# Kernel optimization log

Hardware: AMD Instinct MI355X
Metric: run time of the kernel (lower is better)

The kernel has to match this reference:

```python
import jax, jax.numpy as jnp
import numpy as np

N = 100000
E = 3200000
IN_CH, HID, OUT = 256, 64, 32


def setup_inputs() -> dict:
    key = jax.random.key(0)
    ks = jax.random.split(key, 8)
    x = jax.random.normal(ks[0], (N, IN_CH), dtype=jnp.float32)
    edge_index = jax.random.randint(ks[1], (2, E), 0, N, dtype=jnp.int64)
    # Glorot-ish init for weights, zeros for biases (PyG GCNConv: lin has no bias; conv bias added post-aggregation)
    W1 = jax.random.normal(ks[2], (IN_CH, HID), dtype=jnp.float32) / np.sqrt(IN_CH)
    b1 = jnp.zeros((HID,), dtype=jnp.float32)
    W2 = jax.random.normal(ks[3], (HID, OUT), dtype=jnp.float32) / np.sqrt(HID)
    b2 = jnp.zeros((OUT,), dtype=jnp.float32)
    Wc = jax.random.normal(ks[4], (OUT, 1), dtype=jnp.float32) / np.sqrt(OUT)
    bc = jnp.zeros((1,), dtype=jnp.float32)
    return {"x": x, "edge_index": edge_index, "W1": W1, "b1": b1,
            "W2": W2, "b2": b2, "Wc": Wc, "bc": bc}


def _gcn_norm(edge_index, num_nodes):
    # Add self-loops (PyG default), compute symmetric normalization D^{-1/2} A D^{-1/2}
    loops = jnp.arange(num_nodes, dtype=edge_index.dtype)
    row = jnp.concatenate([edge_index[0], loops])  # source
    col = jnp.concatenate([edge_index[1], loops])  # target (aggregation index)
    ones = jnp.ones(row.shape[0], dtype=jnp.float32)
    deg = jax.ops.segment_sum(ones, col, num_segments=num_nodes)
    dis = jnp.where(deg > 0, jax.lax.rsqrt(jnp.maximum(deg, 1e-12)), 0.0)
    norm = dis[row] * dis[col]  # [E+N]
    return row, col, norm


def _gcn_conv(x, W, b, row, col, norm, num_nodes):
    h = x @ W                                   # [N, F_out] dense transform first
    msg = h[row] * norm[:, None]                # gather + scale per edge
    agg = jax.ops.segment_sum(msg, col, num_segments=num_nodes)
    return agg + b


def reference(x, edge_index, W1, b1, W2, b2, Wc, bc):
    num_nodes = x.shape[0]
    row, col, norm = _gcn_norm(edge_index, num_nodes)
    h = jax.nn.elu(_gcn_conv(x, W1, b1, row, col, norm, num_nodes))
    h = jax.nn.elu(_gcn_conv(h, W2, b2, row, col, norm, num_nodes))
    return (h @ Wc + bc)[:, 0]                  # squeeze(1) -> [N]
```

## Files before the change

### kernel.cpp

```cpp
#include <hip/hip_runtime.h>
#include <hip/hip_fp16.h>
#include <math.h>

#define N_NODES 100000
#define N_EDGES 3200000
#define IN_CH   256
#define HID     64
#define OUTC    32
#define BSHIFT  7
#define BNODES  128
#define NBUCK   ((N_NODES + BNODES - 1) / BNODES)
#define CHUNK   4096
#define EPT     16
#define CAP     4608
#define NPART   ((N_EDGES + CHUNK - 1) / CHUNK)
#define NG1     ((N_NODES + 127) / 128)

static constexpr size_t align256(size_t x) { return (x + 255) & ~(size_t)255; }
static constexpr size_t OFF_PTRB = 0;
static constexpr size_t OFF_PTRE = OFF_PTRB + align256((size_t)N_NODES * 4);
static constexpr size_t OFF_GCUR = OFF_PTRE + align256((size_t)N_NODES * 4);
static constexpr size_t OFF_DIS  = OFF_GCUR + align256((size_t)NBUCK * 4);
static constexpr size_t OFF_SRC  = OFF_DIS  + align256((size_t)N_NODES * 4);
static constexpr size_t OFF_PART = OFF_SRC  + align256((size_t)NBUCK * CAP * 4);
static constexpr size_t OFF_S1   = OFF_PART + align256((size_t)NBUCK * CAP * 4);
static constexpr size_t OFF_S2   = OFF_S1   + align256((size_t)N_NODES * HID * 2);

typedef _Float16 f16;
typedef f16 f16x8 __attribute__((ext_vector_type(8)));
typedef float f32x4 __attribute__((ext_vector_type(4)));

__device__ __forceinline__ void acc8(float* acc, float4 raw) {
    const __half2* hp = (const __half2*)&raw;
    float2 f0 = __half22float2(hp[0]);
    float2 f1 = __half22float2(hp[1]);
    float2 f2 = __half22float2(hp[2]);
    float2 f3 = __half22float2(hp[3]);
    acc[0] += f0.x; acc[1] += f0.y; acc[2] += f1.x; acc[3] += f1.y;
    acc[4] += f2.x; acc[5] += f2.y; acc[6] += f3.x; acc[7] += f3.y;
}


__device__ __forceinline__ void partition_body(int pb, const int* __restrict__ row,
                                               const int* __restrict__ col,
                                               int* __restrict__ gcur,
                                               int* __restrict__ part,
                                               char* smem) {
    int* lhist = (int*)smem;
    int* lbase = lhist + NBUCK;
    const int t  = threadIdx.x;
    const int e0 = pb * CHUNK;
    for (int i = t; i < NBUCK; i += 256) lhist[i] = 0;
    __syncthreads();

    int pk[EPT], br[EPT];
#pragma unroll
    for (int i = 0; i < EPT; ++i) {
        int e = e0 + i * 256 + t;
        if (e < N_EDGES) {
            int d = col[e];
            int b = d >> BSHIFT;
            int r = atomicAdd(&lhist[b], 1);
            pk[i] = row[e] | ((d & (BNODES - 1)) << 17);
            br[i] = b | (r << 10);
        } else {
            br[i] = -1;
        }
    }
    __syncthreads();

    const int off = (int)((pb * 131u) % NBUCK);
    for (int i = t; i < NBUCK; i += 256) {
        int bb = i + off;
        if (bb >= NBUCK) bb -= NBUCK;
        int c = lhist[bb];
        lbase[bb] = (c > 0) ? atomicAdd(&gcur[bb], c) : 0;
    }
    __syncthreads();

#pragma unroll
    for (int i = 0; i < EPT; ++i) {
        if (br[i] >= 0) {
            int b = br[i] & 1023;
            int r = br[i] >> 10;
            part[b * CAP + lbase[b] + r] = pk[i];
        }
    }
}

__device__ __forceinline__ void gemm1_body(int gb, const float* __restrict__ x,
                                           const float* __restrict__ W1,
                                           __half* __restrict__ s1h,
                                           char* lds_raw) {
    f16* xh  = (f16*)lds_raw;
    f16* xl  = (f16*)(lds_raw + 10240);
    f16* wth = (f16*)(lds_raw + 20480);
    f16* wtl = (f16*)(lds_raw + 25600);

    const int t    = threadIdx.x;
    const int row0 = gb * 128;
    const int lane = t & 63;
    const int wv   = t >> 6;
    const int lr   = lane & 15;
    const int kg   = lane >> 4;

    f32x4 acc[2][4];
#pragma unroll
    for (int m = 0; m < 2; ++m)
#pragma unroll
        for (int n = 0; n < 4; ++n) acc[m][n] = (f32x4){0.f, 0.f, 0.f, 0.f};

    for (int kt = 0; kt < 8; ++kt) {
#pragma unroll
        for (int i = 0; i < 4; ++i) {
            int L  = i * 256 + t;
            int r  = L >> 3;
            int k4 = L & 7;
            int rg = row0 + r;
            float4 v = make_float4(0.f, 0.f, 0.f, 0.f);
            if (rg < N_NODES)
                v = ((const float4*)x)[(size_t)rg * 64 + kt * 8 + k4];
            union { f16 h[4]; unsigned long long u; } ph, pl;
            const float* vf = (const float*)&v;
#pragma unroll
            for (int c = 0; c < 4; ++c) {
                f16 hi = (f16)vf[c];
                ph.h[c] = hi;
                pl.h[c] = (f16)(vf[c] - (float)hi);
            }
            *(unsigned long long*)(&xh[r * 40 + k4 * 4]) = ph.u;
            *(unsigned long long*)(&xl[r * 40 + k4 * 4]) = pl.u;
        }
#pragma unroll
        for (int i = 0; i < 2; ++i) {
            int L  = i * 256 + t;
            int k  = L >> 4;
            int j4 = L & 15;
            float4 v = ((const float4*)W1)[(size_t)(kt * 32 + k) * 16 + j4];
            const float* vf = (const float*)&v;
#pragma unroll
            for (int c = 0; c < 4; ++c) {
                f16 hi = (f16)vf[c];
                wth[(j4 * 4 + c) * 40 + k] = hi;
                wtl[(j4 * 4 + c) * 40 + k] = (f16)(vf[c] - (float)hi);
            }
        }
        __syncthreads();

        f16x8 ah[2], al[2], bh[4], bl[4];
#pragma unroll
        for (int m = 0; m < 2; ++m) {
            ah[m] = *(const f16x8*)(&xh[(wv * 32 + m * 16 + lr) * 40 + kg * 8]);
            al[m] = *(const f16x8*)(&xl[(wv * 32 + m * 16 + lr) * 40 + kg * 8]);
        }
#pragma unroll
        for (int n = 0; n < 4; ++n) {
            bh[n] = *(const f16x8*)(&wth[(n * 16 + lr) * 40 + kg * 8]);
            bl[n] = *(const f16x8*)(&wtl[(n * 16 + lr) * 40 + kg * 8]);
        }
#pragma unroll
        for (int m = 0; m < 2; ++m)
#pragma unroll
            for (int n = 0; n < 4; ++n) {
                acc[m][n] = __builtin_amdgcn_mfma_f32_16x16x32_f16(ah[m], bh[n], acc[m][n], 0, 0, 0);
                acc[m][n] = __builtin_amdgcn_mfma_f32_16x16x32_f16(ah[m], bl[n], acc[m][n], 0, 0, 0);
                acc[m][n] = __builtin_amdgcn_mfma_f32_16x16x32_f16(al[m], bh[n], acc[m][n], 0, 0, 0);
            }
        __syncthreads();
    }

    f16* ob = (f16*)lds_raw;
#pragma unroll
    for (int m = 0; m < 2; ++m) {
#pragma unroll
        for (int r = 0; r < 4; ++r) {
            int rl = wv * 32 + m * 16 + kg * 4 + r;
#pragma unroll
            for (int n = 0; n < 4; ++n)
                ob[rl * 72 + n * 16 + lr] = (f16)(acc[m][n][r]);
        }
    }
    __syncthreads();
#pragma unroll
    for (int i = 0; i < 4; ++i) {
        int L = i * 256 + t;
        int r = L >> 3;
        int sg = L & 7;
        int rg = row0 + r;
        if (rg < N_NODES) {
            f16x8 v = *(const f16x8*)(&ob[r * 72 + sg * 8]);
            *(f16x8*)(s1h + (size_t)rg * HID + sg * 8) = v;
        }
    }
}

__global__ __launch_bounds__(256) void fused_pg(const int* __restrict__ row,
                                                const int* __restrict__ col,
                                                int* __restrict__ gcur,
                                                int* __restrict__ part,
                                                const float* __restrict__ x,
                                                const float* __restrict__ W1,
                                                __half* __restrict__ s1h) {
    __shared__ __align__(16) char smem[30720];
    const int bid = blockIdx.x;
    if (bid & 1) gemm1_body(bid >> 1, x, W1, s1h, smem);
    else         partition_body(bid >> 1, row, col, gcur, part, smem);
}

__global__ __launch_bounds__(512) void bucket_build(const int* __restrict__ gcur,
                                                    const int* __restrict__ part,
                                                    int* __restrict__ ptrb,
                                                    int* __restrict__ ptre,
                                                    float* __restrict__ dis,
                                                    int* __restrict__ srcs,
                                                    __half* __restrict__ s1h) {
    __shared__ int pcache[CAP];
    __shared__ int lh[BNODES];
    __shared__ int lb[BNODES];
    __shared__ int lcur[BNODES];
    __shared__ int ls[BNODES];
    __shared__ float ldis[BNODES];
    const int b = blockIdx.x;
    const int t = threadIdx.x;
    if (t < BNODES) { lh[t] = 0; lcur[t] = 0; }
    __syncthreads();
    const int cnt = gcur[b];
    const size_t pbase = (size_t)b * CAP;

    for (int i = t; i < cnt; i += 512) {
        int p = part[pbase + i];
        pcache[i] = p;
        atomicAdd(&lh[p >> 17], 1);
    }
    __syncthreads();

    int val = (t < BNODES) ? lh[t] : 0;
    if (t < BNODES) ls[t] = val;
    __syncthreads();
    for (int off = 1; off < BNODES; off <<= 1) {
        int add = (t >= off && t < BNODES) ? ls[t - off] : 0;
        __syncthreads();
        if (t < BNODES) ls[t] += add;
        __syncthreads();
    }
    if (t < BNODES) lb[t] = ls[t] - val;
    __syncthreads();

    int v = b * BNODES + t;
    if (t < BNODES) {
        float d = rsqrtf((float)val + 1.0f);
        ldis[t] = d;
        if (v < N_NODES) {
            ptrb[v] = b * CAP + lb[t];
            ptre[v] = b * CAP + lb[t] + val;
            dis[v]  = d;
        }
    }
    __syncthreads();

    for (int i = t; i < cnt; i += 512) {
        int p    = pcache[i];
        int dlow = p >> 17;
        int src  = p & 0x1FFFF;
        int r    = atomicAdd(&lcur[dlow], 1);
        srcs[pbase + lb[dlow] + r] = src;
    }

    {
        int nrows = N_NODES - b * BNODES;
        if (nrows > BNODES) nrows = BNODES;
        const int nwork = nrows * 8;
        for (int i = t; i < nwork; i += 512) {
            int r  = i >> 3;
            int sg = i & 7;
            __half* p = s1h + (size_t)(b * BNODES + r) * HID + sg * 8;
            f16x8 vv = *(const f16x8*)p;
            float d = ldis[r];
            f16x8 ov;
#pragma unroll
            for (int c = 0; c < 8; ++c) ov[c] = (f16)((float)vv[c] * d);
            *(f16x8*)p = ov;
        }
    }
}

__global__ __launch_bounds__(256) void gather1(const __half* __restrict__ s1h,
                                               const int* __restrict__ ptrb,
                                               const int* __restrict__ ptre,
                                               const int* __restrict__ srcs,
                                               const float* __restrict__ dis,
                                               const float* __restrict__ b1,
                                               const float* __restrict__ W2,
                                               __half* __restrict__ s2h) {
    __shared__ float w2lds[HID * OUTC];
    __shared__ float hbuf[4][HID];

    const int t = threadIdx.x;
    {
        float4* l4 = (float4*)w2lds;
        const float4* s4 = (const float4*)W2;
        l4[t] = s4[t];
        l4[256 + t] = s4[256 + t];
    }
    __syncthreads();

    const int j = t & 63;
    const int w = t >> 6;
    const int l = j & 31;
    const int h = j >> 5;
    const int v = __builtin_amdgcn_readfirstlane(blockIdx.x * 4 + w);
    const __half2* s12 = (const __half2*)s1h;

    float2 acc;
    {
        float2 self = __half22float2(s12[(v << 5) | l]);
        acc = (h == 0) ? self : make_float2(0.f, 0.f);
    }
    const int beg = ptrb[v];
    const int end = ptre[v];

    for (int base = beg; base < end; base += 64) {
        int mysrc = 0;
        if (base + j < end) mysrc = srcs[base + j];
        int nk = end - base;
        if (nk > 64) nk = 64;
        const int full = nk >> 1;
        int i = 0;
        for (; i + 8 <= full; i += 8) {
            int s  = 2 * i + h;
            int a0 = __shfl(mysrc, s,      64);
            int a1 = __shfl(mysrc, s + 2,  64);
            int a2 = __shfl(mysrc, s + 4,  64);
            int a3 = __shfl(mysrc, s + 6,  64);
            int a4 = __shfl(mysrc, s + 8,  64);
            int a5 = __shfl(mysrc, s + 10, 64);
            int a6 = __shfl(mysrc, s + 12, 64);
            int a7 = __shfl(mysrc, s + 14, 64);
            float2 g0 = __half22float2(s12[(a0 << 5) | l]);
            float2 g1 = __half22float2(s12[(a1 << 5) | l]);
            float2 g2 = __half22float2(s12[(a2 << 5) | l]);
            float2 g3 = __half22float2(s12[(a3 << 5) | l]);
            float2 g4 = __half22float2(s12[(a4 << 5) | l]);
            float2 g5 = __half22float2(s12[(a5 << 5) | l]);
            float2 g6 = __half22float2(s12[(a6 << 5) | l]);
            float2 g7 = __half22float2(s12[(a7 << 5) | l]);
            acc.x += ((g0.x + g1.x) + (g2.x + g3.x)) + ((g4.x + g5.x) + (g6.x + g7.x));
            acc.y += ((g0.y + g1.y) + (g2.y + g3.y)) + ((g4.y + g5.y) + (g6.y + g7.y));
        }
        if (2 * i < nk) {
            const int last = nk - 1;
#pragma unroll
            for (int u = 0; u < 8; ++u) {
                int s  = 2 * (i + u) + h;
                int sc = s < last ? s : last;
                int a  = __shfl(mysrc, sc, 64);
                float wgt = (s < nk) ? 1.f : 0.f;
                float2 g = __half22float2(s12[(a << 5) | l]);
                acc.x = fmaf(wgt, g.x, acc.x);
                acc.y = fmaf(wgt, g.y, acc.y);
            }
        }
    }
    acc.x += __shfl_xor(acc.x, 32, 64);
    acc.y += __shfl_xor(acc.y, 32, 64);

    float dv = dis[v];
    float2 bb = *(const float2*)(b1 + 2 * l);
    float t0 = dv * acc.x + bb.x;
    float t1 = dv * acc.y + bb.y;
    float h0 = t0 > 0.f ? t0 : (expf(t0) - 1.f);
    float h1 = t1 > 0.f ? t1 : (expf(t1) - 1.f);
    if (h == 0) {
        hbuf[w][2 * l]     = h0;
        hbuf[w][2 * l + 1] = h1;
    }

    const int jo = j & 31;
    const int kb = (j >> 5) * 32;
    float p = 0.f;
#pragma unroll
    for (int kk = 0; kk < 32; ++kk)
        p += hbuf[w][kb + kk] * w2lds[(kb + kk) * OUTC + jo];
    p += __shfl_xor(p, 32, 64);
    if (j < 32) {
        s2h[(size_t)v * OUTC + jo] = __float2half(dv * p);
    }
}

__global__ __launch_bounds__(256) void gather2(const __half* __restrict__ s2h,
                                               const int* __restrict__ ptrb,
                                               const int* __restrict__ ptre,
                                               const int* __restrict__ srcs,
                                               const float* __restrict__ dis,
                                               const float* __restrict__ b2,
                                               const float* __restrict__ Wc,
                                               const float* __restrict__ bc,
                                               float* __restrict__ out) {
    const int j = threadIdx.x & 63;
    const int w = threadIdx.x >> 6;
    const int l = j & 3;
    const int e = j >> 2;
    const int v = __builtin_amdgcn_readfirstlane(blockIdx.x * 4 + w);
    const float4* s24 = (const float4*)s2h;

    float acc[8] = {0.f, 0.f, 0.f, 0.f, 0.f, 0.f, 0.f, 0.f};
    if (e == 0) acc8(acc, s24[(v << 2) | l]);

    const int beg = ptrb[v];
    const int end = ptre[v];
    for (int base = beg; base < end; base += 64) {
        int mys = 0;
        if (base + j < end) mys = srcs[base + j];
        int nk = end - base;
        if (nk > 64) nk = 64;
        int off = 0;
        for (; off + 32 <= nk; off += 32) {
            int a0 = __shfl(mys, off + e,      64);
            int a1 = __shfl(mys, off + 16 + e, 64);
            float4 r0 = s24[(a0 << 2) | l];
            float4 r1 = s24[(a1 << 2) | l];
            acc8(acc, r0);
            acc8(acc, r1);
        }
        if (off < nk) {
            const int last = nk - 1;
            int s0 = off + e, s1 = off + 16 + e;
            int a0 = __shfl(mys, s0 < last ? s0 : last, 64);
            int a1 = __shfl(mys, s1 < last ? s1 : last, 64);
            if (s0 < nk) acc8(acc, s24[(a0 << 2) | l]);
            if (s1 < nk) acc8(acc, s24[(a1 << 2) | l]);
        }
    }
#pragma unroll
    for (int i = 0; i < 8; ++i) {
        acc[i] += __shfl_xor(acc[i], 4, 64);
        acc[i] += __shfl_xor(acc[i], 8, 64);
        acc[i] += __shfl_xor(acc[i], 16, 64);
        acc[i] += __shfl_xor(acc[i], 32, 64);
    }

    float dv = dis[v];
    float4 ba = ((const float4*)b2)[2 * l];
    float4 bb = ((const float4*)b2)[2 * l + 1];
    float4 wa = ((const float4*)Wc)[2 * l];
    float4 wb = ((const float4*)Wc)[2 * l + 1];
    const float* bf = (const float*)&ba;
    const float* bg = (const float*)&bb;
    const float* wf = (const float*)&wa;
    const float* wg = (const float*)&wb;
    float p = 0.f;
#pragma unroll
    for (int i = 0; i < 8; ++i) {
        float bias = (i < 4) ? bf[i] : bg[i - 4];
        float wc   = (i < 4) ? wf[i] : wg[i - 4];
        float tt = dv * acc[i] + bias;
        float hh = tt > 0.f ? tt : (expf(tt) - 1.f);
        p += hh * wc;
    }
    p += __shfl_xor(p, 1, 64);
    p += __shfl_xor(p, 2, 64);
    if (j == 0) out[v] = p + bc[0];
}

extern "C" void kernel_launch(void* const* d_in, const int* in_sizes, int n_in,
                              void* d_out, int out_size, void* d_ws, size_t ws_size,
                              hipStream_t stream) {
    const float* x  = (const float*)d_in[0];
    const int*   ei = (const int*)d_in[1];
    const float* W1 = (const float*)d_in[2];
    const float* b1 = (const float*)d_in[3];
    const float* W2 = (const float*)d_in[4];
    const float* b2 = (const float*)d_in[5];
    const float* Wc = (const float*)d_in[6];
    const float* bc = (const float*)d_in[7];
    float* out = (float*)d_out;

    const int* row = ei;
    const int* col = ei + N_EDGES;

    char* ws = (char*)d_ws;
    int*    ptrb = (int*)   (ws + OFF_PTRB);
    int*    ptre = (int*)   (ws + OFF_PTRE);
    int*    gcur = (int*)   (ws + OFF_GCUR);
    float*  dis  = (float*) (ws + OFF_DIS);
    int*    srcs = (int*)   (ws + OFF_SRC);
    int*    part = (int*)   (ws + OFF_PART);
    __half* s1h  = (__half*)(ws + OFF_S1);
    __half* s2h  = (__half*)(ws + OFF_S2);

    hipMemsetAsync(gcur, 0, (size_t)NBUCK * 4, stream);
    fused_pg    <<<NPART + NG1, 256, 0, stream>>>(row, col, gcur, part, x, W1, s1h);
    bucket_build<<<NBUCK, 512, 0, stream>>>(gcur, part, ptrb, ptre, dis, srcs, s1h);

    gather1<<<N_NODES / 4, 256, 0, stream>>>(s1h, ptrb, ptre, srcs, dis, b1, W2, s2h);
    gather2<<<N_NODES / 4, 256, 0, stream>>>(s2h, ptrb, ptre, srcs, dis, b2, Wc, bc, out);
}
```

Measured before the change: 363.2 us.

## Fuse bucket build and both gather passes into one cooperative persistent kernel

Replaces the separate bucket_build, gather1 and gather2 launches with a single cooperative persistent kernel. Phases are separated by grid-wide syncs, and each phase uses grid-stride loops over buckets and nodes. The bucket build now uses per-wave histograms so the LDS atomics contend less. This removes two kernel launch boundaries and tail effects. In exchange it adds grid-sync cost, and the grid is capped at 1024 blocks of 512 threads with launch bounds of 6, which may limit occupancy for the latency-bound gathers.

```diff
diff --git a/kernel.cpp b/kernel.cpp
--- a/kernel.cpp
+++ b/kernel.cpp
@@ -1,6 +1,9 @@
 #include <hip/hip_runtime.h>
+#include <hip/hip_cooperative_groups.h>
 #include <hip/hip_fp16.h>
 #include <math.h>
+
+namespace cg = cooperative_groups;
 
 #define N_NODES 100000
 #define N_EDGES 3200000
@@ -40,7 +43,6 @@
     acc[4] += f2.x; acc[5] += f2.y; acc[6] += f3.x; acc[7] += f3.y;
 }
 
-
 __device__ __forceinline__ void partition_body(int pb, const int* __restrict__ row,
                                                const int* __restrict__ col,
                                                int* __restrict__ gcur,
@@ -207,259 +209,260 @@
     else         partition_body(bid >> 1, row, col, gcur, part, smem);
 }
 
-__global__ __launch_bounds__(512) void bucket_build(const int* __restrict__ gcur,
-                                                    const int* __restrict__ part,
-                                                    int* __restrict__ ptrb,
-                                                    int* __restrict__ ptre,
-                                                    float* __restrict__ dis,
-                                                    int* __restrict__ srcs,
-                                                    __half* __restrict__ s1h) {
-    __shared__ int pcache[CAP];
-    __shared__ int lh[BNODES];
-    __shared__ int lb[BNODES];
-    __shared__ int lcur[BNODES];
-    __shared__ int ls[BNODES];
-    __shared__ float ldis[BNODES];
-    const int b = blockIdx.x;
-    const int t = threadIdx.x;
-    if (t < BNODES) { lh[t] = 0; lcur[t] = 0; }
+__global__ __launch_bounds__(512, 6) void tail_fused(
+        const int* __restrict__ gcur, const int* __restrict__ part,
+        int* __restrict__ ptrb, int* __restrict__ ptre,
+        float* __restrict__ dis, int* __restrict__ srcs,
+        __half* __restrict__ s1h, __half* __restrict__ s2h,
+        const float* __restrict__ b1, const float* __restrict__ W2,
+        const float* __restrict__ b2, const float* __restrict__ Wc,
+        const float* __restrict__ bc, float* __restrict__ out) {
+    __shared__ __align__(16) char sm[27776];
+    int*   pcache = (int*)sm;
+    int*   wh     = (int*)(sm + 18432);
+    int*   wpre   = (int*)(sm + 22656);
+    int*   lsm    = (int*)(sm + 26752);
+    float* ldis   = (float*)(sm + 27264);
+    float* w2lds  = (float*)sm;
+    float* hbuf   = (float*)(sm + 8192);
+
+    const int t  = threadIdx.x;
+    const int wv = t >> 6;
+    const int j  = t & 63;
+
+    for (int b = blockIdx.x; b < NBUCK; b += gridDim.x) {
+        const int cnt = gcur[b];
+        const size_t pbase = (size_t)b * CAP;
+
+        for (int i = t; i < 8 * 132; i += 512) wh[i] = 0;
+        __syncthreads();
+
+        for (int i = t; i < cnt; i += 512) {
+            int p = part[pbase + i];
+            pcache[i] = p;
+            atomicAdd(&wh[wv * 132 + (p >> 17)], 1);
+        }
+        __syncthreads();
+
+        int val = 0, lbv = 0;
+        if (t < BNODES) {
+            int s = 0;
+#pragma unroll
+            for (int q = 0; q < 8; ++q) { wpre[q * 128 + t] = s; s += wh[q * 132 + t]; }
+            val = s;
+            lsm[t] = s;
+        }
+        __syncthreads();
+        for (int off = 1; off < BNODES; off <<= 1) {
+            int add = (t >= off && t < BNODES) ? lsm[t - off] : 0;
+            __syncthreads();
+            if (t < BNODES) lsm[t] += add;
+            __syncthreads();
+        }
+        if (t < BNODES) {
+            lbv = lsm[t] - val;
+            float d = rsqrtf((float)val + 1.0f);
+            ldis[t] = d;
+            int v = b * BNODES + t;
+            if (v < N_NODES) {
+                ptrb[v] = b * CAP + lbv;
+                ptre[v] = b * CAP + lbv + val;
+                dis[v]  = d;
+            }
+#pragma unroll
+            for (int q = 0; q < 8; ++q) wh[q * 132 + t] = lbv + wpre[q * 128 + t];
+        }
+        __syncthreads();
+
+        for (int i = t; i < cnt; i += 512) {
+            int p    = pcache[i];
+            int dlow = p >> 17;
+            int r    = atomicAdd(&wh[wv * 132 + dlow], 1);
+            srcs[pbase + r] = p & 0x1FFFF;
+        }
+
+        {
+            int base_node = b * BNODES;
+            int nrows = N_NODES - base_node;
+            if (nrows > BNODES) nrows = BNODES;
+            int nwork = nrows * 8;
+            for (int i = t; i < nwork; i += 512) {
+                int r  = i >> 3;
+                int sg = i & 7;
+                f16x8* pp = (f16x8*)(s1h + (size_t)(base_node + r) * HID + sg * 8);
+                f16x8 vv = *pp;
+                float d = ldis[r];
+                f16x8 ov;
+#pragma unroll
+                for (int c = 0; c < 8; ++c) ov[c] = (f16)((float)vv[c] * d);
+                *pp = ov;
+            }
+        }
+        __syncthreads();
+    }
+
+    __threadfence();
+    cg::this_grid().sync();
+
+    {
+        const float4* s4 = (const float4*)W2;
+        if (t < 512) ((float4*)w2lds)[t] = s4[t];
+    }
     __syncthreads();
-    const int cnt = gcur[b];
-    const size_t pbase = (size_t)b * CAP;
-
-    for (int i = t; i < cnt; i += 512) {
-        int p = part[pbase + i];
-        pcache[i] = p;
-        atomicAdd(&lh[p >> 17], 1);
-    }
-    __syncthreads();
-
-    int val = (t < BNODES) ? lh[t] : 0;
-    if (t < BNODES) ls[t] = val;
-    __syncthreads();
-    for (int off = 1; off < BNODES; off <<= 1) {
-        int add = (t >= off && t < BNODES) ? ls[t - off] : 0;
-        __syncthreads();
-        if (t < BNODES) ls[t] += add;
-        __syncthreads();
-    }
-    if (t < BNODES) lb[t] = ls[t] - val;
-    __syncthreads();
-
-    int v = b * BNODES + t;
-    if (t < BNODES) {
-        float d = rsqrtf((float)val + 1.0f);
-        ldis[t] = d;
-        if (v < N_NODES) {
-            ptrb[v] = b * CAP + lb[t];
-            ptre[v] = b * CAP + lb[t] + val;
-            dis[v]  = d;
-        }
-    }
-    __syncthreads();
-
-    for (int i = t; i < cnt; i += 512) {
-        int p    = pcache[i];
-        int dlow = p >> 17;
-        int src  = p & 0x1FFFF;
-        int r    = atomicAdd(&lcur[dlow], 1);
-        srcs[pbase + lb[dlow] + r] = src;
-    }
 
     {
-        int nrows = N_NODES - b * BNODES;
-        if (nrows > BNODES) nrows = BNODES;
-        const int nwork = nrows * 8;
-        for (int i = t; i < nwork; i += 512) {
-            int r  = i >> 3;
-            int sg = i & 7;
-            __half* p = s1h + (size_t)(b * BNODES + r) * HID + sg * 8;
-            f16x8 vv = *(const f16x8*)p;
-            float d = ldis[r];
-            f16x8 ov;
-#pragma unroll
-            for (int c = 0; c < 8; ++c) ov[c] = (f16)((float)vv[c] * d);
-            *(f16x8*)p = ov;
-        }
-    }
-}
-
-__global__ __launch_bounds__(256) void gather1(const __half* __restrict__ s1h,
-                                               const int* __restrict__ ptrb,
-                                               const int* __restrict__ ptre,
-                                               const int* __restrict__ srcs,
-                                               const float* __restrict__ dis,
-                                               const float* __restrict__ b1,
-                                               const float* __restrict__ W2,
-                                               __half* __restrict__ s2h) {
-    __shared__ float w2lds[HID * OUTC];
-    __shared__ float hbuf[4][HID];
-
-    const int t = threadIdx.x;
+        const int l = j & 31;
+        const int h = j >> 5;
+        const __half2* s12 = (const __half2*)s1h;
+        const int nw = gridDim.x * 8;
+        for (int vv = blockIdx.x * 8 + wv; vv < N_NODES; vv += nw) {
+            const int v = __builtin_amdgcn_readfirstlane(vv);
+            float2 acc;
+            {
+                float2 self = __half22float2(s12[(v << 5) | l]);
+                acc = (h == 0) ? self : make_float2(0.f, 0.f);
+            }
+            const int beg = ptrb[v];
+            const int end = ptre[v];
+
+            for (int base = beg; base < end; base += 64) {
+                int mysrc = 0;
+                if (base + j < end) mysrc = srcs[base + j];
+                int nk = end - base;
+                if (nk > 64) nk = 64;
+                const int full = nk >> 1;
+                int i = 0;
+                for (; i + 8 <= full; i += 8) {
+                    int s  = 2 * i + h;
+                    int a0 = __shfl(mysrc, s,      64);
+                    int a1 = __shfl(mysrc, s + 2,  64);
+                    int a2 = __shfl(mysrc, s + 4,  64);
+                    int a3 = __shfl(mysrc, s + 6,  64);
+                    int a4 = __shfl(mysrc, s + 8,  64);
+                    int a5 = __shfl(mysrc, s + 10, 64);
+                    int a6 = __shfl(mysrc, s + 12, 64);
+                    int a7 = __shfl(mysrc, s + 14, 64);
+                    float2 g0 = __half22float2(s12[(a0 << 5) | l]);
+                    float2 g1 = __half22float2(s12[(a1 << 5) | l]);
+                    float2 g2 = __half22float2(s12[(a2 << 5) | l]);
+                    float2 g3 = __half22float2(s12[(a3 << 5) | l]);
+                    float2 g4 = __half22float2(s12[(a4 << 5) | l]);
+                    float2 g5 = __half22float2(s12[(a5 << 5) | l]);
+                    float2 g6 = __half22float2(s12[(a6 << 5) | l]);
+                    float2 g7 = __half22float2(s12[(a7 << 5) | l]);
+                    acc.x += ((g0.x + g1.x) + (g2.x + g3.x)) + ((g4.x + g5.x) + (g6.x + g7.x));
+                    acc.y += ((g0.y + g1.y) + (g2.y + g3.y)) + ((g4.y + g5.y) + (g6.y + g7.y));
+                }
+                if (2 * i < nk) {
+                    const int last = nk - 1;
+#pragma unroll
+                    for (int u = 0; u < 8; ++u) {
+                        int s  = 2 * (i + u) + h;
+                        int sc = s < last ? s : last;
+                        int a  = __shfl(mysrc, sc, 64);
+                        float wgt = (s < nk) ? 1.f : 0.f;
+                        float2 g = __half22float2(s12[(a << 5) | l]);
+                        acc.x = fmaf(wgt, g.x, acc.x);
+                        acc.y = fmaf(wgt, g.y, acc.y);
+                    }
+                }
+            }
+            acc.x += __shfl_xor(acc.x, 32, 64);
+            acc.y += __shfl_xor(acc.y, 32, 64);
+
+            float dv = dis[v];
+            float2 bb = *(const float2*)(b1 + 2 * l);
+            float t0 = dv * acc.x + bb.x;
+            float t1 = dv * acc.y + bb.y;
+            float h0 = t0 > 0.f ? t0 : (expf(t0) - 1.f);
+            float h1 = t1 > 0.f ? t1 : (expf(t1) - 1.f);
+            if (h == 0) {
+                hbuf[wv * HID + 2 * l]     = h0;
+                hbuf[wv * HID + 2 * l + 1] = h1;
+            }
+
+            const int jo = j & 31;
+            const int kb = (j >> 5) * 32;
+            float p = 0.f;
+#pragma unroll
+            for (int kk = 0; kk < 32; ++kk)
+                p += hbuf[wv * HID + kb + kk] * w2lds[(kb + kk) * OUTC + jo];
+            p += __shfl_xor(p, 32, 64);
+            if (j < 32) {
+                s2h[(size_t)v * OUTC + jo] = __float2half(dv * p);
+            }
+        }
+    }
+
+    __threadfence();
+    cg::this_grid().sync();
+
     {
-        float4* l4 = (float4*)w2lds;
-        const float4* s4 = (const float4*)W2;
-        l4[t] = s4[t];
-        l4[256 + t] = s4[256 + t];
-    }
-    __syncthreads();
-
-    const int j = t & 63;
-    const int w = t >> 6;
-    const int l = j & 31;
-    const int h = j >> 5;
-    const int v = __builtin_amdgcn_readfirstlane(blockIdx.x * 4 + w);
-    const __half2* s12 = (const __half2*)s1h;
-
-    float2 acc;
-    {
-        float2 self = __half22float2(s12[(v << 5) | l]);
-        acc = (h == 0) ? self : make_float2(0.f, 0.f);
-    }
-    const int beg = ptrb[v];
-    const int end = ptre[v];
-
-    for (int base = beg; base < end; base += 64) {
-        int mysrc = 0;
-        if (base + j < end) mysrc = srcs[base + j];
-        int nk = end - base;
-        if (nk > 64) nk = 64;
-        const int full = nk >> 1;
-        int i = 0;
-        for (; i + 8 <= full; i += 8) {
-            int s  = 2 * i + h;
-            int a0 = __shfl(mysrc, s,      64);
-            int a1 = __shfl(mysrc, s + 2,  64);
-            int a2 = __shfl(mysrc, s + 4,  64);
-            int a3 = __shfl(mysrc, s + 6,  64);
-            int a4 = __shfl(mysrc, s + 8,  64);
-            int a5 = __shfl(mysrc, s + 10, 64);
-            int a6 = __shfl(mysrc, s + 12, 64);
-            int a7 = __shfl(mysrc, s + 14, 64);
-            float2 g0 = __half22float2(s12[(a0 << 5) | l]);
-            float2 g1 = __half22float2(s12[(a1 << 5) | l]);
-            float2 g2 = __half22float2(s12[(a2 << 5) | l]);
-            float2 g3 = __half22float2(s12[(a3 << 5) | l]);
-            float2 g4 = __half22float2(s12[(a4 << 5) | l]);
-            float2 g5 = __half22float2(s12[(a5 << 5) | l]);
-            float2 g6 = __half22float2(s12[(a6 << 5) | l]);
-            float2 g7 = __half22float2(s12[(a7 << 5) | l]);
-            acc.x += ((g0.x + g1.x) + (g2.x + g3.x)) + ((g4.x + g5.x) + (g6.x + g7.x));
-            acc.y += ((g0.y + g1.y) + (g2.y + g3.y)) + ((g4.y + g5.y) + (g6.y + g7.y));
-        }
-        if (2 * i < nk) {
-            const int last = nk - 1;
-#pragma unroll
-            for (int u = 0; u < 8; ++u) {
-                int s  = 2 * (i + u) + h;
-                int sc = s < last ? s : last;
-                int a  = __shfl(mysrc, sc, 64);
-                float wgt = (s < nk) ? 1.f : 0.f;
-                float2 g = __half22float2(s12[(a << 5) | l]);
-                acc.x = fmaf(wgt, g.x, acc.x);
-                acc.y = fmaf(wgt, g.y, acc.y);
-            }
-        }
-    }
-    acc.x += __shfl_xor(acc.x, 32, 64);
-    acc.y += __shfl_xor(acc.y, 32, 64);
-
-    float dv = dis[v];
-    float2 bb = *(const float2*)(b1 + 2 * l);
-    float t0 = dv * acc.x + bb.x;
-    float t1 = dv * acc.y + bb.y;
-    float h0 = t0 > 0.f ? t0 : (expf(t0) - 1.f);
-    float h1 = t1 > 0.f ? t1 : (expf(t1) - 1.f);
-    if (h == 0) {
-        hbuf[w][2 * l]     = h0;
-        hbuf[w][2 * l + 1] = h1;
-    }
-
-    const int jo = j & 31;
-    const int kb = (j >> 5) * 32;
-    float p = 0.f;
-#pragma unroll
-    for (int kk = 0; kk < 32; ++kk)
-        p += hbuf[w][kb + kk] * w2lds[(kb + kk) * OUTC + jo];
-    p += __shfl_xor(p, 32, 64);
-    if (j < 32) {
-        s2h[(size_t)v * OUTC + jo] = __float2half(dv * p);
-    }
-}
-
-__global__ __launch_bounds__(256) void gather2(const __half* __restrict__ s2h,
-                                               const int* __restrict__ ptrb,
-                                               const int* __restrict__ ptre,
-                                               const int* __restrict__ srcs,
-                                               const float* __restrict__ dis,
-                                               const float* __restrict__ b2,
-                                               const float* __restrict__ Wc,
-                                               const float* __restrict__ bc,
-                                               float* __restrict__ out) {
-    const int j = threadIdx.x & 63;
-    const int w = threadIdx.x >> 6;
-    const int l = j & 3;
-    const int e = j >> 2;
-    const int v = __builtin_amdgcn_readfirstlane(blockIdx.x * 4 + w);
-    const float4* s24 = (const float4*)s2h;
-
-    float acc[8] = {0.f, 0.f, 0.f, 0.f, 0.f, 0.f, 0.f, 0.f};
-    if (e == 0) acc8(acc, s24[(v << 2) | l]);
-
-    const int beg = ptrb[v];
-    const int end = ptre[v];
-    for (int base = beg; base < end; base += 64) {
-        int mys = 0;
-        if (base + j < end) mys = srcs[base + j];
-        int nk = end - base;
-        if (nk > 64) nk = 64;
-        int off = 0;
-        for (; off + 32 <= nk; off += 32) {
-            int a0 = __shfl(mys, off + e,      64);
-            int a1 = __shfl(mys, off + 16 + e, 64);
-            float4 r0 = s24[(a0 << 2) | l];
-            float4 r1 = s24[(a1 << 2) | l];
-            acc8(acc, r0);
-            acc8(acc, r1);
-        }
-        if (off < nk) {
-            const int last = nk - 1;
-            int s0 = off + e, s1 = off + 16 + e;
-            int a0 = __shfl(mys, s0 < last ? s0 : last, 64);
-            int a1 = __shfl(mys, s1 < last ? s1 : last, 64);
-            if (s0 < nk) acc8(acc, s24[(a0 << 2) | l]);
-            if (s1 < nk) acc8(acc, s24[(a1 << 2) | l]);
-        }
-    }
-#pragma unroll
-    for (int i = 0; i < 8; ++i) {
-        acc[i] += __shfl_xor(acc[i], 4, 64);
-        acc[i] += __shfl_xor(acc[i], 8, 64);
-        acc[i] += __shfl_xor(acc[i], 16, 64);
-        acc[i] += __shfl_xor(acc[i], 32, 64);
-    }
-
-    float dv = dis[v];
-    float4 ba = ((const float4*)b2)[2 * l];
-    float4 bb = ((const float4*)b2)[2 * l + 1];
-    float4 wa = ((const float4*)Wc)[2 * l];
-    float4 wb = ((const float4*)Wc)[2 * l + 1];
-    const float* bf = (const float*)&ba;
-    const float* bg = (const float*)&bb;
-    const float* wf = (const float*)&wa;
-    const float* wg = (const float*)&wb;
-    float p = 0.f;
-#pragma unroll
-    for (int i = 0; i < 8; ++i) {
-        float bias = (i < 4) ? bf[i] : bg[i - 4];
-        float wc   = (i < 4) ? wf[i] : wg[i - 4];
-        float tt = dv * acc[i] + bias;
-        float hh = tt > 0.f ? tt : (expf(tt) - 1.f);
-        p += hh * wc;
-    }
-    p += __shfl_xor(p, 1, 64);
-    p += __shfl_xor(p, 2, 64);
-    if (j == 0) out[v] = p + bc[0];
+        const int l = j & 3;
+        const int e = j >> 2;
+        const float4* s24 = (const float4*)s2h;
+        const int nw = gridDim.x * 8;
+        for (int vv = blockIdx.x * 8 + wv; vv < N_NODES; vv += nw) {
+            const int v = __builtin_amdgcn_readfirstlane(vv);
+            float acc[8] = {0.f, 0.f, 0.f, 0.f, 0.f, 0.f, 0.f, 0.f};
+            if (e == 0) acc8(acc, s24[(v << 2) | l]);
+
+            const int beg = ptrb[v];
+            const int end = ptre[v];
+            for (int base = beg; base < end; base += 64) {
+                int mys = 0;
+                if (base + j < end) mys = srcs[base + j];
+                int nk = end - base;
+                if (nk > 64) nk = 64;
+                int off = 0;
+                for (; off + 32 <= nk; off += 32) {
+                    int a0 = __shfl(mys, off + e,      64);
+                    int a1 = __shfl(mys, off + 16 + e, 64);
+                    float4 r0 = s24[(a0 << 2) | l];
+                    float4 r1 = s24[(a1 << 2) | l];
+                    acc8(acc, r0);
+                    acc8(acc, r1);
+                }
+                if (off < nk) {
+                    const int last = nk - 1;
+                    int s0 = off + e, s1 = off + 16 + e;
+                    int a0 = __shfl(mys, s0 < last ? s0 : last, 64);
+                    int a1 = __shfl(mys, s1 < last ? s1 : last, 64);
+                    if (s0 < nk) acc8(acc, s24[(a0 << 2) | l]);
+                    if (s1 < nk) acc8(acc, s24[(a1 << 2) | l]);
+                }
+            }
+#pragma unroll
+            for (int i = 0; i < 8; ++i) {
+                acc[i] += __shfl_xor(acc[i], 4, 64);
+                acc[i] += __shfl_xor(acc[i], 8, 64);
+                acc[i] += __shfl_xor(acc[i], 16, 64);
+                acc[i] += __shfl_xor(acc[i], 32, 64);
+            }
+
+            float dv = dis[v];
+            float4 ba = ((const float4*)b2)[2 * l];
+            float4 bb = ((const float4*)b2)[2 * l + 1];
+            float4 wa = ((const float4*)Wc)[2 * l];
+            float4 wb = ((const float4*)Wc)[2 * l + 1];
+            const float* bf = (const float*)&ba;
+            const float* bg = (const float*)&bb;
+            const float* wf = (const float*)&wa;
+            const float* wg = (const float*)&wb;
+            float p = 0.f;
+#pragma unroll
+            for (int i = 0; i < 8; ++i) {
+                float bias = (i < 4) ? bf[i] : bg[i - 4];
+                float wc   = (i < 4) ? wf[i] : wg[i - 4];
+                float tt = dv * acc[i] + bias;
+                float hh = tt > 0.f ? tt : (expf(tt) - 1.f);
+                p += hh * wc;
+            }
+            p += __shfl_xor(p, 1, 64);
+            p += __shfl_xor(p, 2, 64);
+            if (j == 0) out[v] = p + bc[0];
+        }
+    }
 }
 
 extern "C" void kernel_launch(void* const* d_in, const int* in_sizes, int n_in,
@@ -489,9 +492,20 @@
     __half* s2h  = (__half*)(ws + OFF_S2);
 
     hipMemsetAsync(gcur, 0, (size_t)NBUCK * 4, stream);
-    fused_pg    <<<NPART + NG1, 256, 0, stream>>>(row, col, gcur, part, x, W1, s1h);
-    bucket_build<<<NBUCK, 512, 0, stream>>>(gcur, part, ptrb, ptre, dis, srcs, s1h);
-
-    gather1<<<N_NODES / 4, 256, 0, stream>>>(s1h, ptrb, ptre, srcs, dis, b1, W2, s2h);
-    gather2<<<N_NODES / 4, 256, 0, stream>>>(s2h, ptrb, ptre, srcs, dis, b2, Wc, bc, out);
+    fused_pg<<<NPART + NG1, 256, 0, stream>>>(row, col, gcur, part, x, W1, s1h);
+
+    static int coop_blocks = 0;
+    if (coop_blocks == 0) {
+        int maxb = 0;
+        hipOccupancyMaxActiveBlocksPerMultiprocessor(&maxb, tail_fused, 512, 0);
+        if (maxb < 1) maxb = 1;
+        coop_blocks = maxb * 256;
+        if (coop_blocks > 1024) coop_blocks = 1024;
+    }
+    void* kargs[] = { (void*)&gcur, (void*)&part, (void*)&ptrb, (void*)&ptre,
+                      (void*)&dis,  (void*)&srcs, (void*)&s1h,  (void*)&s2h,
+                      (void*)&b1,   (void*)&W2,   (void*)&b2,   (void*)&Wc,
+                      (void*)&bc,   (void*)&out };
+    hipLaunchCooperativeKernel((void*)tail_fused, dim3(coop_blocks), dim3(512),
+                               kargs, 0, stream);
 }
```

Result: slower. 755.1 us (+107.9%).
